# Performance work log

Hardware: AMD Instinct MI355X
Metric: run time of the kernel (lower is better)

The kernel has to match this reference:

```python
import jax, jax.numpy as jnp
import numpy as np

B, C, H, W = 128, 2048, 11, 11
BN_EPS = 1e-5
STEEPNESS = 10.0


def setup_inputs() -> dict:
    key = jax.random.key(0)
    ks = jax.random.split(key, 4)
    x = jax.random.normal(ks[0], (B, C, H, W), dtype=jnp.float32)
    freq_threshold = jnp.full((1, C, 1, 1), 0.25, dtype=jnp.float32)
    gate = jnp.full((1,), 0.1, dtype=jnp.float32)
    # kaiming normal fan_out for 1x1 conv: std = sqrt(2 / fan_out), fan_out = C*1*1
    conv_w = jax.random.normal(ks[1], (C, C), dtype=jnp.float32) * np.sqrt(2.0 / C).astype(np.float32)
    conv_b = jnp.zeros((C,), dtype=jnp.float32)
    bn_gamma = jnp.ones((C,), dtype=jnp.float32)
    bn_beta = jnp.zeros((C,), dtype=jnp.float32)
    bn_mean = jnp.zeros((C,), dtype=jnp.float32)
    bn_var = jnp.ones((C,), dtype=jnp.float32)
    return {
        "x": x, "freq_threshold": freq_threshold, "gate": gate,
        "conv_w": conv_w, "conv_b": conv_b,
        "bn_gamma": bn_gamma, "bn_beta": bn_beta,
        "bn_mean": bn_mean, "bn_var": bn_var,
    }


def _hp_mask(cutoff, h, w, dtype):
    # radial distance from the (shifted) DC bin, normalized by max corner distance
    cy, cx = h // 2, w // 2
    yy = (jnp.arange(h, dtype=dtype) - cy)[:, None]
    xx = (jnp.arange(w, dtype=dtype) - cx)[None, :]
    dist = jnp.sqrt(yy ** 2 + xx ** 2)
    max_dist = jnp.sqrt(jnp.asarray(cy ** 2 + cx ** 2, dtype=dtype))
    dn = dist / (max_dist + 1e-6)  # [H, W]
    return jax.nn.sigmoid(STEEPNESS * (dn[None, None] - cutoff))  # [1, C, H, W]


def reference(x, freq_threshold, gate, conv_w, conv_b, bn_gamma, bn_beta, bn_mean, bn_var):
    # FFT -> shifted high-pass mask -> iFFT (real part)
    x_freq = jnp.fft.fftshift(jnp.fft.fft2(x, norm="ortho"), axes=(-2, -1))
    cutoff = jnp.clip(freq_threshold, 0.05, 0.5)
    mask = _hp_mask(cutoff, x.shape[-2], x.shape[-1], x.dtype)
    x_filt = jnp.fft.ifft2(jnp.fft.ifftshift(x_freq * mask, axes=(-2, -1)), norm="ortho").real
    # refine: 1x1 conv + BN (inference stats) + ReLU
    y = jnp.einsum("bchw,oc->bohw", x_filt, conv_w) + conv_b[None, :, None, None]
    inv = (bn_gamma / jnp.sqrt(bn_var + BN_EPS))[None, :, None, None]
    y = (y - bn_mean[None, :, None, None]) * inv + bn_beta[None, :, None, None]
    y = jax.nn.relu(y)
    g = jnp.clip(gate, 0.0, 1.0)
    return x + g * y
```

## Files before the change

kernel.cpp:

```cpp
#include <hip/hip_runtime.h>
#include <cstdint>
#include <cstddef>


#define C_DIM 2048
#define HW 121
#define NB 128
#define NTOT (NB * HW)

__device__ __forceinline__ unsigned short f2bf(float f) {
  union { float f; unsigned int u; } v;
  v.f = f;
  unsigned int r = (v.u + 0x7FFFu + ((v.u >> 16) & 1u)) >> 16;
  return (unsigned short)r;
}

typedef __bf16 bfrag __attribute__((ext_vector_type(8)));
typedef float f32x4 __attribute__((ext_vector_type(4)));

__device__ __forceinline__ void gload_lds16(const void* g, void* l) {
  __builtin_amdgcn_global_load_lds(
      (const __attribute__((address_space(1))) unsigned int*)(uintptr_t)g,
      (__attribute__((address_space(3))) unsigned int*)(uintptr_t)l, 16, 0, 0);
}

__global__ __launch_bounds__(256) void prep_kernel(
    const float* __restrict__ ft, const float* __restrict__ convb,
    const float* __restrict__ gamma, const float* __restrict__ beta,
    const float* __restrict__ mean, const float* __restrict__ var,
    const float* __restrict__ W, unsigned short* __restrict__ Wb,
    float* __restrict__ kws, float* __restrict__ alpha,
    float* __restrict__ beta2) {
  __shared__ float msk[121];
  __shared__ float ctab[11];
  const int c = blockIdx.x;
  const int t = threadIdx.x;

  {
    int base = c * C_DIM + t * 8;
    float4 a = *(const float4*)(W + base);
    float4 b = *(const float4*)(W + base + 4);
    union { unsigned short s[8]; uint4 v; } u;
    u.s[0] = f2bf(a.x); u.s[1] = f2bf(a.y); u.s[2] = f2bf(a.z); u.s[3] = f2bf(a.w);
    u.s[4] = f2bf(b.x); u.s[5] = f2bf(b.y); u.s[6] = f2bf(b.z); u.s[7] = f2bf(b.w);
    *(uint4*)(Wb + base) = u.v;
  }

  float cutoff = ft[c];
  cutoff = fminf(fmaxf(cutoff, 0.05f), 0.5f);
  if (t < 121) {
    int h = t / 11, w = t - (t / 11) * 11;
    float dy = (float)(h - 5), dx = (float)(w - 5);
    float dn = sqrtf(dy * dy + dx * dx) / (sqrtf(50.0f) + 1e-6f);
    msk[t] = 1.0f / (1.0f + expf(-10.0f * (dn - cutoff)));
  }
  if (t < 11) ctab[t] = cosf(6.283185307179586f * (float)t / 11.0f);
  if (t == 128) {
    float inv = gamma[c] * rsqrtf(var[c] + 1e-5f);
    alpha[c] = inv;
    beta2[c] = (convb[c] - mean[c]) * inv + beta[c];
  }
  __syncthreads();
  if (t < 176) {
    int h = t >> 4, w = t & 15;
    float val = 0.0f;
    if (w < 11) {
      float acc = 0.0f;
      int ru = 0;
      int us = 5;
      for (int u = 0; u < 11; u++) {
        int rv = ru;
        int vs = 5;
        for (int v = 0; v < 11; v++) {
          acc += msk[us * 11 + vs] * ctab[rv];
          rv += w; if (rv >= 11) rv -= 11;
          vs++; if (vs >= 11) vs -= 11;
        }
        ru += h; if (ru >= 11) ru -= 11;
        us++; if (us >= 11) us -= 11;
      }
      val = acc * (1.0f / 121.0f);
    }
    kws[(size_t)c * 176 + t] = val;
  }
}

#define XROW 12
#define XPL 132
#define FC 32
__global__ __launch_bounds__(384) void filter_kernel(
    const float* __restrict__ x, const float* __restrict__ kws,
    unsigned short* __restrict__ xf) {
  __shared__ __align__(16) float lx[FC * XPL];
  __shared__ __align__(16) unsigned short lo[HW * FC];
  const int b = blockIdx.x;
  const int c0 = blockIdx.y * FC;
  const int tid = threadIdx.x;

  const float* xsrc = x + ((size_t)b * C_DIM + c0) * HW;
#pragma unroll
  for (int i = 0; i < 3; i++) {
    int v = tid + i * 384;
    if (v < 968) {
      float4 xv = *(const float4*)(xsrc + v * 4);
      int g = v * 4;
#pragma unroll
      for (int e = 0; e < 4; e++) {
        int ge = g + e;
        int pl = ge / 121;
        int r = ge - pl * 121;
        int rh = r / 11;
        int rw = r - rh * 11;
        lx[pl * XPL + rh * XROW + rw] = (&xv.x)[e];
      }
    }
  }
  __syncthreads();

  if (tid < 352) {
    const int pl = tid / 11;
    const int ph = tid - pl * 11;
    const float* xp = &lx[pl * XPL];
    const float* kp = kws + (size_t)(c0 + pl) * 176;

    float accv[11];
#pragma unroll
    for (int i = 0; i < 11; i++) accv[i] = 0.f;

#pragma unroll
    for (int d = 0; d <= 5; d++) {
      int q0 = ph - d; if (q0 < 0) q0 += 11;
      f32x4 r0 = *(const f32x4*)(xp + q0 * XROW);
      f32x4 r1 = *(const f32x4*)(xp + q0 * XROW + 4);
      f32x4 r2 = *(const f32x4*)(xp + q0 * XROW + 8);
      if (d > 0) {
        int q1 = ph + d; if (q1 >= 11) q1 -= 11;
        r0 += *(const f32x4*)(xp + q1 * XROW);
        r1 += *(const f32x4*)(xp + q1 * XROW + 4);
        r2 += *(const f32x4*)(xp + q1 * XROW + 8);
      }
      const float R[11] = {r0[0], r0[1], r0[2], r0[3], r1[0], r1[1],
                           r1[2], r1[3], r2[0], r2[1], r2[2]};
      f32x4 k0 = *(const f32x4*)(kp + d * 16);
      f32x4 k1 = *(const f32x4*)(kp + d * 16 + 4);
      f32x4 k2 = *(const f32x4*)(kp + d * 16 + 8);
      const float K[11] = {k0[0], k0[1], k0[2], k0[3], k1[0], k1[1],
                           k1[2], k1[3], k2[0], k2[1], k2[2]};
#pragma unroll
      for (int qw = 0; qw < 11; qw++) {
#pragma unroll
        for (int pw = 0; pw < 11; pw++) {
          int ki = pw - qw; if (ki < 0) ki += 11;
          accv[pw] = fmaf(R[qw], K[ki], accv[pw]);
        }
      }
    }
#pragma unroll
    for (int pw = 0; pw < 11; pw++)
      lo[(ph * 11 + pw) * FC + pl] = f2bf(accv[pw]);
  }
  __syncthreads();

  const unsigned int* lou = (const unsigned int*)lo;
#pragma unroll
  for (int i = 0; i < 6; i++) {
    int idx = tid + i * 384;
    if (idx < 1936) {
      int p = idx >> 4;
      int j = idx & 15;
      ((unsigned int*)(xf + (size_t)(b * HW + p) * C_DIM + c0))[j] = lou[idx];
    }
  }
}

__global__ __launch_bounds__(256) void gemm_kernel(
    const unsigned short* __restrict__ Wb, const unsigned short* __restrict__ xf,
    const float* __restrict__ xres, const float* __restrict__ alpha,
    const float* __restrict__ beta2, const float* __restrict__ gate,
    float* __restrict__ out) {
  __shared__ __align__(16) unsigned short lds[16384];
  const int tid = threadIdx.x;
  const int wid = tid >> 6;
  const int lane = tid & 63;

  const int lid = blockIdx.y * 121 + blockIdx.x;
  const int grp = lid / 176;
  const int rem = lid - grp * 176;
  const int m0 = (rem & 15) << 7;
  const int n0 = (grp * 11 + (rem >> 4)) << 7;

  const int wm = (wid >> 1) << 6;
  const int wn = (wid & 1) << 6;

  f32x4 acc[4][4];
#pragma unroll
  for (int i = 0; i < 4; i++)
#pragma unroll
    for (int j = 0; j < 4; j++) acc[i][j] = f32x4{0.f, 0.f, 0.f, 0.f};

  const int rowlo = (wid << 4) + (lane >> 2);
  const int seg = lane & 3;
  const unsigned short* gA0 = Wb + (size_t)(m0 + rowlo) * C_DIM + seg * 8;
  const unsigned short* gA1 = gA0 + 64 * C_DIM;
  const unsigned short* gB0 = xf + (size_t)(n0 + rowlo) * C_DIM + seg * 8;
  const unsigned short* gB1 = gB0 + 64 * C_DIM;
  char* lA0 = (char*)lds + (wid << 10) + (lane << 4);
  char* lA1 = lA0 + 4096;

  const int fr = lane & 15;
  const int quad = lane >> 4;
  const unsigned short* pa = lds + ((wm + fr) << 5) + (quad << 3);
  const unsigned short* pb = lds + 8192 + ((wn + fr) << 5) + (quad << 3);

  for (int kk = 0; kk < 32; kk++) {
    gload_lds16(gA0,       lA0);
    gload_lds16(gA1,       lA1);
    gload_lds16(gA0 + 32,  lA0 + 8192);
    gload_lds16(gA1 + 32,  lA1 + 8192);
    gload_lds16(gB0,       lA0 + 16384);
    gload_lds16(gB1,       lA1 + 16384);
    gload_lds16(gB0 + 32,  lA0 + 24576);
    gload_lds16(gB1 + 32,  lA1 + 24576);
    gA0 += 64; gA1 += 64; gB0 += 64; gB1 += 64;
    asm volatile("s_waitcnt vmcnt(0)" ::: "memory");
    __syncthreads();
#pragma unroll
    for (int ks = 0; ks < 2; ks++) {
      bfrag a[4], b[4];
#pragma unroll
      for (int i = 0; i < 4; i++) {
        a[i] = *(const bfrag*)(pa + (ks << 12) + (i << 9));
        b[i] = *(const bfrag*)(pb + (ks << 12) + (i << 9));
      }
#pragma unroll
      for (int i = 0; i < 4; i++)
#pragma unroll
        for (int j = 0; j < 4; j++)
          acc[i][j] = __builtin_amdgcn_mfma_f32_16x16x32_bf16(a[i], b[j], acc[i][j], 0, 0, 0);
    }
    __syncthreads();
  }

  float g = gate[0];
  g = fminf(fmaxf(g, 0.0f), 1.0f);
  int nbase[4];
#pragma unroll
  for (int j = 0; j < 4; j++) {
    int n = n0 + wn + (j << 4) + fr;
    int bb = n / 121;
    int p = n - bb * 121;
    nbase[j] = bb * (C_DIM * HW) + p;
  }
#pragma unroll
  for (int i = 0; i < 4; i++) {
    const int ob = m0 + wm + (i << 4) + (quad << 2);
    float al[4], bt[4];
#pragma unroll
    for (int r = 0; r < 4; r++) { al[r] = alpha[ob + r]; bt[r] = beta2[ob + r]; }
#pragma unroll
    for (int j = 0; j < 4; j++) {
#pragma unroll
      for (int r = 0; r < 4; r++) {
        int addr = nbase[j] + (ob + r) * HW;
        float v = acc[i][j][r] * al[r] + bt[r];
        v = fmaxf(v, 0.0f);
        out[addr] = xres[addr] + g * v;
      }
    }
  }
}

extern "C" void kernel_launch(void* const* d_in, const int* in_sizes, int n_in,
                              void* d_out, int out_size, void* d_ws, size_t ws_size,
                              hipStream_t stream) {
  const float* x     = (const float*)d_in[0];
  const float* ft    = (const float*)d_in[1];
  const float* gate  = (const float*)d_in[2];
  const float* W     = (const float*)d_in[3];
  const float* convb = (const float*)d_in[4];
  const float* gamma = (const float*)d_in[5];
  const float* beta  = (const float*)d_in[6];
  const float* mean  = (const float*)d_in[7];
  const float* var   = (const float*)d_in[8];
  float* out = (float*)d_out;

  char* ws = (char*)d_ws;
  float* kws            = (float*)(ws);
  float* alpha          = (float*)(ws + 0x200000);
  float* beta2          = (float*)(ws + 0x202000);
  unsigned short* Wb    = (unsigned short*)(ws + 0x300000);
  unsigned short* xf    = (unsigned short*)(ws + 0xC00000);

  prep_kernel<<<2048, 256, 0, stream>>>(ft, convb, gamma, beta, mean, var,
                                        W, Wb, kws, alpha, beta2);
  filter_kernel<<<dim3(NB, C_DIM / FC), 384, 0, stream>>>(x, kws, xf);
  gemm_kernel<<<dim3(NTOT / 128, C_DIM / 128), 256, 0, stream>>>(
      Wb, xf, x, alpha, beta2, gate, out);
}
```

Before: 472.4 us.

## Replace GEMM with 256x256-tile double-buffered, swizzled, ping-pong scheduled kernel

```diff
diff --git a/kernel.cpp b/kernel.cpp
--- a/kernel.cpp
+++ b/kernel.cpp
@@ -18,7 +18,7 @@
 typedef __bf16 bfrag __attribute__((ext_vector_type(8)));
 typedef float f32x4 __attribute__((ext_vector_type(4)));
 
-__device__ __forceinline__ void gload_lds16(const void* g, void* l) {
+__device__ __forceinline__ void gload16(const unsigned short* g, char* l) {
   __builtin_amdgcn_global_load_lds(
       (const __attribute__((address_space(1))) unsigned int*)(uintptr_t)g,
       (__attribute__((address_space(3))) unsigned int*)(uintptr_t)l, 16, 0, 0);
@@ -173,101 +173,182 @@
   }
 }
 
-__global__ __launch_bounds__(256) void gemm_kernel(
+
+#define SCHED __builtin_amdgcn_sched_barrier(0)
+#define BAR do { SCHED; __builtin_amdgcn_s_barrier(); SCHED; } while (0)
+#define LGKM0 do { asm volatile("s_waitcnt lgkmcnt(0)" ::: "memory"); SCHED; } while (0)
+#define VM0 asm volatile("s_waitcnt vmcnt(0)" ::: "memory")
+#define P1 __builtin_amdgcn_s_setprio(1)
+#define P0 __builtin_amdgcn_s_setprio(0)
+
+#define RDA(BUF, MH) do { \
+  const char* _pa = pa0 + (BUF)*65536 + (MH)*16384; \
+  _Pragma("unroll") \
+  for (int _i = 0; _i < 4; ++_i) { \
+    a[_i][0] = *(const bfrag*)(_pa + _i*2048 + sx0); \
+    a[_i][1] = *(const bfrag*)(_pa + _i*2048 + sx1); \
+  } } while (0)
+
+#define RDB(BUF, NH) do { \
+  const char* _pb = pb0 + (BUF)*65536 + (NH)*4096; \
+  _Pragma("unroll") \
+  for (int _j = 0; _j < 2; ++_j) { \
+    b[(NH)*2+_j][0] = *(const bfrag*)(_pb + _j*2048 + sx0); \
+    b[(NH)*2+_j][1] = *(const bfrag*)(_pb + _j*2048 + sx1); \
+  } } while (0)
+
+#define MM(MH, NH) do { \
+  _Pragma("unroll") \
+  for (int _i = 0; _i < 4; ++_i) { \
+    _Pragma("unroll") \
+    for (int _j = 0; _j < 2; ++_j) { \
+      f32x4 _c = acc[(MH)*4+_i][(NH)*2+_j]; \
+      _c = __builtin_amdgcn_mfma_f32_16x16x32_bf16(a[_i][0], b[(NH)*2+_j][0], _c, 0, 0, 0); \
+      _c = __builtin_amdgcn_mfma_f32_16x16x32_bf16(a[_i][1], b[(NH)*2+_j][1], _c, 0, 0, 0); \
+      acc[(MH)*4+_i][(NH)*2+_j] = _c; \
+    } } } while (0)
+
+__global__ __launch_bounds__(512, 2) void gemm256_kernel(
     const unsigned short* __restrict__ Wb, const unsigned short* __restrict__ xf,
     const float* __restrict__ xres, const float* __restrict__ alpha,
     const float* __restrict__ beta2, const float* __restrict__ gate,
     float* __restrict__ out) {
-  __shared__ __align__(16) unsigned short lds[16384];
+  __shared__ __align__(16) unsigned short lds[65536];
   const int tid = threadIdx.x;
+  const int lane = tid & 63;
   const int wid = tid >> 6;
-  const int lane = tid & 63;
-
-  const int lid = blockIdx.y * 121 + blockIdx.x;
-  const int grp = lid / 176;
-  const int rem = lid - grp * 176;
-  const int m0 = (rem & 15) << 7;
-  const int n0 = (grp * 11 + (rem >> 4)) << 7;
-
-  const int wm = (wid >> 1) << 6;
-  const int wn = (wid & 1) << 6;
-
-  f32x4 acc[4][4];
-#pragma unroll
-  for (int i = 0; i < 4; i++)
-#pragma unroll
-    for (int j = 0; j < 4; j++) acc[i][j] = f32x4{0.f, 0.f, 0.f, 0.f};
-
-  const int rowlo = (wid << 4) + (lane >> 2);
-  const int seg = lane & 3;
-  const unsigned short* gA0 = Wb + (size_t)(m0 + rowlo) * C_DIM + seg * 8;
-  const unsigned short* gA1 = gA0 + 64 * C_DIM;
-  const unsigned short* gB0 = xf + (size_t)(n0 + rowlo) * C_DIM + seg * 8;
-  const unsigned short* gB1 = gB0 + 64 * C_DIM;
-  char* lA0 = (char*)lds + (wid << 10) + (lane << 4);
-  char* lA1 = lA0 + 4096;
-
   const int fr = lane & 15;
   const int quad = lane >> 4;
-  const unsigned short* pa = lds + ((wm + fr) << 5) + (quad << 3);
-  const unsigned short* pb = lds + 8192 + ((wn + fr) << 5) + (quad << 3);
-
-  for (int kk = 0; kk < 32; kk++) {
-    gload_lds16(gA0,       lA0);
-    gload_lds16(gA1,       lA1);
-    gload_lds16(gA0 + 32,  lA0 + 8192);
-    gload_lds16(gA1 + 32,  lA1 + 8192);
-    gload_lds16(gB0,       lA0 + 16384);
-    gload_lds16(gB1,       lA1 + 16384);
-    gload_lds16(gB0 + 32,  lA0 + 24576);
-    gload_lds16(gB1 + 32,  lA1 + 24576);
-    gA0 += 64; gA1 += 64; gB0 += 64; gB1 += 64;
-    asm volatile("s_waitcnt vmcnt(0)" ::: "memory");
-    __syncthreads();
-#pragma unroll
-    for (int ks = 0; ks < 2; ks++) {
-      bfrag a[4], b[4];
-#pragma unroll
-      for (int i = 0; i < 4; i++) {
-        a[i] = *(const bfrag*)(pa + (ks << 12) + (i << 9));
-        b[i] = *(const bfrag*)(pb + (ks << 12) + (i << 9));
-      }
-#pragma unroll
-      for (int i = 0; i < 4; i++)
-#pragma unroll
-        for (int j = 0; j < 4; j++)
-          acc[i][j] = __builtin_amdgcn_mfma_f32_16x16x32_bf16(a[i], b[j], acc[i][j], 0, 0, 0);
-    }
-    __syncthreads();
+  const int wrow = wid >> 2;
+  const int wcol = wid & 3;
+
+  const int bid = blockIdx.x;
+  const int wg = (bid & 7) * 61 + (bid >> 3);
+  const int m0 = (wg & 7) << 8;
+  const int n0 = (wg >> 3) << 8;
+
+  const int rowoff = tid >> 3;
+  const int sg8 = ((tid & 7) ^ ((tid >> 3) & 7)) << 3;
+  const unsigned short* pA00 = Wb + (size_t)(m0 + rowoff) * C_DIM + sg8;
+  const unsigned short* pA01 = Wb + (size_t)(m0 + 128 + rowoff) * C_DIM + sg8;
+  const unsigned short* pA10 = Wb + (size_t)(m0 + 64 + rowoff) * C_DIM + sg8;
+  const unsigned short* pA11 = Wb + (size_t)(m0 + 192 + rowoff) * C_DIM + sg8;
+  int nr0 = n0 + rowoff;        if (nr0 > NTOT - 1) nr0 = NTOT - 1;
+  int nr1 = n0 + 64 + rowoff;   if (nr1 > NTOT - 1) nr1 = NTOT - 1;
+  int nr2 = n0 + 128 + rowoff;  if (nr2 > NTOT - 1) nr2 = NTOT - 1;
+  int nr3 = n0 + 192 + rowoff;  if (nr3 > NTOT - 1) nr3 = NTOT - 1;
+  const unsigned short* pB00 = xf + (size_t)nr0 * C_DIM + sg8;
+  const unsigned short* pB01 = xf + (size_t)nr1 * C_DIM + sg8;
+  const unsigned short* pB10 = xf + (size_t)nr2 * C_DIM + sg8;
+  const unsigned short* pB11 = xf + (size_t)nr3 * C_DIM + sg8;
+
+  char* Lc = (char*)lds;
+  char* Ld = Lc + tid * 16;
+
+  const int fx = fr & 7;
+  const int sx0 = ((quad ^ fx) << 4);
+  const int sx1 = (((4 + quad) ^ fx) << 4);
+  const char* pa0 = Lc + (wrow << 13) + (fr << 7);
+  const char* pb0 = Lc + 32768 + (wcol << 13) + (fr << 7);
+
+  f32x4 acc[8][4];
+#pragma unroll
+  for (int i = 0; i < 8; ++i)
+#pragma unroll
+    for (int j = 0; j < 4; ++j) acc[i][j] = f32x4{0.f, 0.f, 0.f, 0.f};
+  bfrag a[4][2], b[4][2];
+
+#define G16(P, OFFB, LOFF) \
+  gload16((const unsigned short*)((const char*)(P) + (OFFB)), Ld + (LOFF))
+#define ISS1 do { G16(pA10, 128, 65536+16384); G16(pA11, 128, 65536+16384+8192); } while (0)
+#define ISS2 do { G16(pA00, 256, 0);           G16(pA01, 256, 8192); } while (0)
+#define ISS3 do { G16(pB00, 256, 32768);       G16(pB01, 256, 32768+8192); } while (0)
+#define ISS4 do { G16(pB10, 256, 32768+16384); G16(pB11, 256, 32768+16384+8192); } while (0)
+#define ISS5 do { G16(pA10, 256, 16384);       G16(pA11, 256, 16384+8192); } while (0)
+#define ISS6 do { G16(pA00, 384, 65536);       G16(pA01, 384, 65536+8192); } while (0)
+#define ISS7 do { G16(pB00, 384, 65536+32768); G16(pB01, 384, 65536+32768+8192); } while (0)
+#define ISS8 do { G16(pB10, 384, 65536+32768+16384); G16(pB11, 384, 65536+32768+16384+8192); } while (0)
+
+  G16(pA00, 0, 0);               G16(pA01, 0, 8192);
+  G16(pA10, 0, 16384);           G16(pA11, 0, 16384+8192);
+  G16(pB00, 0, 32768);           G16(pB01, 0, 32768+8192);
+  G16(pB10, 0, 32768+16384);     G16(pB11, 0, 32768+16384+8192);
+  SCHED;
+  VM0;
+  SCHED;
+  G16(pA00, 128, 65536);         G16(pA01, 128, 65536+8192);
+  G16(pB00, 128, 65536+32768);   G16(pB01, 128, 65536+32768+8192);
+  G16(pB10, 128, 65536+32768+16384); G16(pB11, 128, 65536+32768+16384+8192);
+  SCHED;
+  BAR;
+
+#pragma unroll 1
+  for (int it = 0; it < 16; ++it) {
+    const bool full = (it < 15);
+    RDA(0, 0); RDB(0, 0);
+    ISS1;
+    BAR; LGKM0; P1; MM(0, 0); P0; BAR;
+    RDB(0, 1);
+    if (full) ISS2;
+    BAR; LGKM0; P1; MM(0, 1); P0; BAR;
+    RDA(0, 1);
+    if (full) ISS3;
+    BAR; LGKM0; P1; MM(1, 0); P0; BAR;
+    SCHED; VM0; SCHED;
+    if (full) ISS4;
+    BAR; LGKM0; P1; MM(1, 1); P0; BAR;
+    RDA(1, 0); RDB(1, 0);
+    if (full) ISS5;
+    BAR; LGKM0; P1; MM(0, 0); P0; BAR;
+    RDB(1, 1);
+    if (full) ISS6;
+    BAR; LGKM0; P1; MM(0, 1); P0; BAR;
+    RDA(1, 1);
+    if (full) ISS7;
+    BAR; LGKM0; P1; MM(1, 0); P0; BAR;
+    SCHED; VM0; SCHED;
+    if (full) ISS8;
+    BAR; LGKM0; P1; MM(1, 1); P0; BAR;
+    pA00 += 128; pA01 += 128; pA10 += 128; pA11 += 128;
+    pB00 += 128; pB01 += 128; pB10 += 128; pB11 += 128;
   }
 
   float g = gate[0];
   g = fminf(fmaxf(g, 0.0f), 1.0f);
-  int nbase[4];
-#pragma unroll
-  for (int j = 0; j < 4; j++) {
-    int n = n0 + wn + (j << 4) + fr;
-    int bb = n / 121;
-    int p = n - bb * 121;
-    nbase[j] = bb * (C_DIM * HW) + p;
-  }
-#pragma unroll
-  for (int i = 0; i < 4; i++) {
-    const int ob = m0 + wm + (i << 4) + (quad << 2);
-    float al[4], bt[4];
-#pragma unroll
-    for (int r = 0; r < 4; r++) { al[r] = alpha[ob + r]; bt[r] = beta2[ob + r]; }
-#pragma unroll
-    for (int j = 0; j < 4; j++) {
-#pragma unroll
-      for (int r = 0; r < 4; r++) {
-        int addr = nbase[j] + (ob + r) * HW;
-        float v = acc[i][j][r] * al[r] + bt[r];
-        v = fmaxf(v, 0.0f);
-        out[addr] = xres[addr] + g * v;
-      }
-    }
-  }
+  int nb[4];
+  bool nv[4];
+#pragma unroll
+  for (int nh = 0; nh < 2; ++nh)
+#pragma unroll
+    for (int j = 0; j < 2; ++j) {
+      const int idx = nh * 2 + j;
+      int n = n0 + wcol * 64 + nh * 32 + j * 16 + fr;
+      nv[idx] = (n < NTOT);
+      int bb = n / 121;
+      int p = n - bb * 121;
+      if (!nv[idx]) { bb = 0; p = 0; }
+      nb[idx] = bb * (C_DIM * HW) + p;
+    }
+#pragma unroll
+  for (int mh = 0; mh < 2; ++mh)
+#pragma unroll
+    for (int i2 = 0; i2 < 4; ++i2) {
+      const int ob = m0 + wrow * 128 + mh * 64 + i2 * 16 + quad * 4;
+      const float4 al = *(const float4*)(alpha + ob);
+      const float4 bt = *(const float4*)(beta2 + ob);
+#pragma unroll
+      for (int idx = 0; idx < 4; ++idx) {
+        if (nv[idx]) {
+#pragma unroll
+          for (int rr = 0; rr < 4; ++rr) {
+            int addr = nb[idx] + (ob + rr) * HW;
+            float v = acc[mh * 4 + i2][idx][rr] * (&al.x)[rr] + (&bt.x)[rr];
+            v = fmaxf(v, 0.0f);
+            out[addr] = xres[addr] + g * v;
+          }
+        }
+      }
+    }
 }
 
 extern "C" void kernel_launch(void* const* d_in, const int* in_sizes, int n_in,
@@ -294,6 +375,5 @@
   prep_kernel<<<2048, 256, 0, stream>>>(ft, convb, gamma, beta, mean, var,
                                         W, Wb, kws, alpha, beta2);
   filter_kernel<<<dim3(NB, C_DIM / FC), 384, 0, stream>>>(x, kws, xf);
-  gemm_kernel<<<dim3(NTOT / 128, C_DIM / 128), 256, 0, stream>>>(
-      Wb, xf, x, alpha, beta2, gate, out);
-}
+  gemm256_kernel<<<dim3(488), 512, 0, stream>>>(Wb, xf, x, alpha, beta2, gate, out);
+}
```

Measured after the change: 459.5 us. 2.7% less time.
